# Kernel optimization log

Hardware: AMD Instinct MI355X
Metric: run time of the kernel (lower is better)

Reference implementation:

```python
import jax, jax.numpy as jnp
import numpy as np

D = 512        # model dim
NH = 8         # heads
NL = 4         # layers
MSL = 2048     # max_seq_len for relative positional bias
ITEM_V, CATE_V, SEG_V = 100000, 1000, 2
EPS = 1e-5


def layer_norm(x, w, b):
    mu = jnp.mean(x, axis=-1, keepdims=True)
    var = jnp.mean((x - mu) ** 2, axis=-1, keepdims=True)
    return (x - mu) * jax.lax.rsqrt(var + EPS) * w + b


def setup_inputs() -> dict:
    key = jax.random.key(0)
    ks = jax.random.split(key, 16)
    B, L = 8, 1023
    inp = {
        'historical_item_ids': jax.random.randint(ks[0], (B, L), 0, ITEM_V, dtype=jnp.int32),
        'historical_cate_ids': jax.random.randint(ks[1], (B, L), 0, CATE_V, dtype=jnp.int32),
        'historical_len': jax.random.randint(ks[2], (B,), 0, L, dtype=jnp.int32),
        'target_item_id': jax.random.randint(ks[3], (B,), 0, ITEM_V, dtype=jnp.int32),
        'target_cate_id': jax.random.randint(ks[4], (B,), 0, CATE_V, dtype=jnp.int32),
        # embeddings (init std 0.02 like _init_weights)
        'item_emb': 0.02 * jax.random.normal(ks[5], (ITEM_V, D), jnp.float32),
        'cate_emb': 0.02 * jax.random.normal(ks[6], (CATE_V, D), jnp.float32),
        'seg_emb': 0.02 * jax.random.normal(ks[7], (SEG_V, D), jnp.float32),
        # per-layer stacked params
        'W1': 0.02 * jax.random.normal(ks[8], (NL, D, 4 * D), jnp.float32),
        'b1': jnp.zeros((NL, 4 * D), jnp.float32),
        'W2': 0.02 * jax.random.normal(ks[9], (NL, D, D), jnp.float32),
        'b2': jnp.zeros((NL, D), jnp.float32),
        'ln1_w': jnp.ones((NL, D), jnp.float32), 'ln1_b': jnp.zeros((NL, D), jnp.float32),
        'ln2_w': jnp.ones((NL, D), jnp.float32), 'ln2_b': jnp.zeros((NL, D), jnp.float32),
        'pos_w': 0.02 * jax.random.normal(ks[10], (NL, 2 * MSL - 1), jnp.float32),
        'lnf_w': jnp.ones((D,), jnp.float32), 'lnf_b': jnp.zeros((D,), jnp.float32),
    }
    return inp


def _forward(historical_item_ids, historical_cate_ids, historical_len,
             target_item_id, target_cate_id,
             item_emb, cate_emb, seg_emb, W1, b1, W2, b2,
             ln1_w, ln1_b, ln2_w, ln2_b, pos_w, lnf_w, lnf_b):
    B = historical_item_ids.shape[0]
    ar = jnp.arange(B)
    pad = jnp.zeros((B, 1), historical_item_ids.dtype)
    ids = jnp.concatenate([historical_item_ids, pad], axis=1).at[ar, historical_len].set(target_item_id)
    cids = jnp.concatenate([historical_cate_ids, pad], axis=1).at[ar, historical_len].set(target_cate_id)
    S = ids.shape[1]
    seg = jnp.zeros_like(ids).at[ar, historical_len].set(1)

    h = item_emb[ids] + cate_emb[cids] + seg_emb[seg]  # [B,S,D]

    # relative position bias indices: bias[i,j] = pos_w[MSL-1 + j - i]
    rel_idx = MSL - 1 + jnp.arange(S)[None, :] - jnp.arange(S)[:, None]  # [S,S]
    causal = jnp.tril(jnp.ones((S, S), h.dtype))  # multiplicative mask (mask >= 0)

    for l in range(NL):
        z = jax.nn.silu(h @ W1[l] + b1[l])  # [B,S,4D]
        u, q, k, v = jnp.split(z, 4, axis=-1)
        resh = lambda t: t.reshape(B, S, NH, D // NH).transpose(0, 2, 1, 3)  # [B,H,S,hd]
        u, q, k, v = resh(u), resh(q), resh(k), resh(v)
        bias = pos_w[l][rel_idx]  # [S,S]
        att = jax.nn.silu(jnp.einsum('bhsd,bhtd->bhst', q, k) + bias) * causal
        y = jnp.einsum('bhst,bhtd->bhsd', att, v) * u
        y = y.transpose(0, 2, 1, 3).reshape(B, S, D)
        y = layer_norm(y, ln1_w[l], ln1_b[l])
        y = y @ W2[l] + b2[l]
        h = layer_norm(y + h, ln2_w[l], ln2_b[l])  # dropout p=0 (eval)

    return layer_norm(h, lnf_w, lnf_b)


def reference(historical_item_ids, historical_cate_ids, historical_len,
              target_item_id, target_cate_id,
              item_emb, cate_emb, seg_emb, W1, b1, W2, b2,
              ln1_w, ln1_b, ln2_w, ln2_b, pos_w, lnf_w, lnf_b):
    return _forward(historical_item_ids, historical_cate_ids, historical_len,
                    target_item_id, target_cate_id,
                    item_emb, cate_emb, seg_emb, W1, b1, W2, b2,
                    ln1_w, ln1_b, ln2_w, ln2_b, pos_w, lnf_w, lnf_b)
```

## Files before the change

### kernel.cpp

```cpp
#include <hip/hip_runtime.h>
#include <cstddef>


#define D_MODEL 512
#define S_LEN 1024
#define NHEADS 8

typedef __bf16 bf16x8 __attribute__((ext_vector_type(8)));
typedef float f32x4 __attribute__((ext_vector_type(4)));
typedef unsigned short us4 __attribute__((ext_vector_type(4)));
typedef unsigned short us8 __attribute__((ext_vector_type(8)));

__device__ __forceinline__ float silu_f(float x) {
  return x / (1.f + __expf(-x));
}
__device__ __forceinline__ unsigned short f2bf(float f) {
  unsigned int u = __float_as_uint(f);
  u += 0x7FFF + ((u >> 16) & 1);
  return (unsigned short)(u >> 16);
}
__device__ __forceinline__ float bf2f(unsigned short s) {
  return __uint_as_float(((unsigned int)s) << 16);
}
__device__ __forceinline__ void gll16(const void* g, void* l) {
  __builtin_amdgcn_global_load_lds(
      (const __attribute__((address_space(1))) unsigned int*)g,
      (__attribute__((address_space(3))) unsigned int*)l, 16, 0, 0);
}

__global__ __launch_bounds__(256) void embed_kernel(
    const int* __restrict__ hist_i, const int* __restrict__ hist_c,
    const int* __restrict__ hlen, const int* __restrict__ tgt_i,
    const int* __restrict__ tgt_c, const float* __restrict__ item_emb,
    const float* __restrict__ cate_emb, const float* __restrict__ seg_emb,
    float* __restrict__ h32, unsigned short* __restrict__ hbf) {
  int bs = blockIdx.x;
  int b = bs >> 10, s = bs & 1023;
  int l = hlen[b];
  int id, cid, sg;
  if (s == l)       { id = tgt_i[b]; cid = tgt_c[b]; sg = 1; }
  else if (s < 1023){ id = hist_i[b * 1023 + s]; cid = hist_c[b * 1023 + s]; sg = 0; }
  else              { id = 0; cid = 0; sg = 0; }
  const float* ie = item_emb + (size_t)id * D_MODEL;
  const float* ce = cate_emb + (size_t)cid * D_MODEL;
  const float* se = seg_emb + (size_t)sg * D_MODEL;
  float* hr = h32 + (size_t)bs * D_MODEL;
  unsigned short* hb = hbf + (size_t)bs * D_MODEL;
  for (int d = threadIdx.x; d < D_MODEL; d += 256) {
    float v = ie[d] + ce[d] + se[d];
    hr[d] = v;
    hb[d] = f2bf(v);
  }
}

__global__ __launch_bounds__(256) void transpose_kernel(
    const float* __restrict__ W, unsigned short* __restrict__ Wt,
    int K, int N) {
  const int l = blockIdx.z;
  W += (size_t)l * K * N;
  Wt += (size_t)l * K * N;
  const int n0 = blockIdx.x * 64, k0 = blockIdx.y * 64;
  __shared__ float T[64][65];
  const int tid = threadIdx.x;
  const int rr = tid >> 4, cc = (tid & 15) * 4;
#pragma unroll
  for (int p = 0; p < 4; p++) {
    const int r = rr + p * 16;
    const float4 v = *reinterpret_cast<const float4*>(&W[(size_t)(k0 + r) * N + n0 + cc]);
    T[r][cc] = v.x; T[r][cc + 1] = v.y; T[r][cc + 2] = v.z; T[r][cc + 3] = v.w;
  }
  __syncthreads();
#pragma unroll
  for (int p = 0; p < 4; p++) {
    const int r = rr + p * 16;
    us4 o = { f2bf(T[cc + 0][r]), f2bf(T[cc + 1][r]),
              f2bf(T[cc + 2][r]), f2bf(T[cc + 3][r]) };
    *reinterpret_cast<us4*>(&Wt[(size_t)(n0 + r) * K + k0 + cc]) = o;
  }
}

template <int TM, int TN, int EPI_SILU, typename OutT>
__global__ __launch_bounds__(256) void mfma_gemm(
    const unsigned short* __restrict__ A, const unsigned short* __restrict__ Bt,
    const float* __restrict__ bias, OutT* __restrict__ C,
    int M, int N, int K) {
  constexpr int MI = TM / 32, NI = TN / 32;
  __shared__ unsigned short As[TM * 64];
  __shared__ unsigned short Bs[TN * 64];
  const int tid = threadIdx.x;
  const int w = tid >> 6, lane = tid & 63, lm = lane & 15, quad = lane >> 4;
  const int wm = w & 1, wn = w >> 1;
  const int m0 = blockIdx.y * TM, n0 = blockIdx.x * TN;

  f32x4 acc[MI][NI] = {};

  for (int k0 = 0; k0 < K; k0 += 64) {
#pragma unroll
    for (int p = 0; p < TM / 32; p++) {
      const int g = p * 256 + tid;
      const int r = g >> 3;
      const int lc = (g & 7) ^ (r & 7);
      gll16(A + (size_t)(m0 + r) * K + k0 + lc * 8, &As[g * 8]);
    }
#pragma unroll
    for (int p = 0; p < TN / 32; p++) {
      const int g = p * 256 + tid;
      const int r = g >> 3;
      const int lc = (g & 7) ^ (r & 7);
      gll16(Bt + (size_t)(n0 + r) * K + k0 + lc * 8, &Bs[g * 8]);
    }
    __syncthreads();
#pragma unroll
    for (int ki = 0; ki < 2; ki++) {
      bf16x8 af[MI], bfr[NI];
#pragma unroll
      for (int mi = 0; mi < MI; mi++) {
        const int r = wm * (TM / 2) + mi * 16 + lm;
        const int p = (ki * 4 + quad) ^ (lm & 7);
        af[mi] = *reinterpret_cast<const bf16x8*>(&As[r * 64 + p * 8]);
      }
#pragma unroll
      for (int ni = 0; ni < NI; ni++) {
        const int r = wn * (TN / 2) + ni * 16 + lm;
        const int p = (ki * 4 + quad) ^ (lm & 7);
        bfr[ni] = *reinterpret_cast<const bf16x8*>(&Bs[r * 64 + p * 8]);
      }
#pragma unroll
      for (int mi = 0; mi < MI; mi++)
#pragma unroll
        for (int ni = 0; ni < NI; ni++)
          acc[mi][ni] = __builtin_amdgcn_mfma_f32_16x16x32_bf16(
              af[mi], bfr[ni], acc[mi][ni], 0, 0, 0);
    }
    __syncthreads();
  }

#pragma unroll
  for (int ni = 0; ni < NI; ni++) {
    const int n = n0 + wn * (TN / 2) + ni * 16 + lm;
    const float bv = bias[n];
#pragma unroll
    for (int mi = 0; mi < MI; mi++) {
      const int mbase = m0 + wm * (TM / 2) + mi * 16 + quad * 4;
#pragma unroll
      for (int reg = 0; reg < 4; reg++) {
        float v = acc[mi][ni][reg] + bv;
        if (EPI_SILU) v = silu_f(v);
        if constexpr (sizeof(OutT) == 2)
          C[(size_t)(mbase + reg) * N + n] = f2bf(v);
        else
          C[(size_t)(mbase + reg) * N + n] = v;
      }
    }
  }
}

#define LDR 72
__global__ __launch_bounds__(256) void attn_kernel(
    const unsigned short* __restrict__ z, const float* __restrict__ posw,
    float* __restrict__ y) {
  const int qt = blockIdx.x, hh = blockIdx.y, b = blockIdx.z;
  const int s0 = qt * 128;
  __shared__ alignas(16) unsigned short Qs[128 * LDR];
  __shared__ alignas(16) unsigned short Ps[128 * LDR];
  __shared__ alignas(16) unsigned short Ks[64 * LDR];
  __shared__ alignas(16) unsigned short Vt[64 * LDR];
  __shared__ float bias_s[192];
  const unsigned short* zb = z + (size_t)b * S_LEN * 2048;
  const int tid = threadIdx.x;
  const int w = tid >> 6, lane = tid & 63, lm = lane & 15, quad = lane >> 4;

#pragma unroll
  for (int p = 0; p < 4; p++) {
    const int g = p * 256 + tid;
    const int r = g >> 3, ch = (g & 7) * 8;
    *reinterpret_cast<us8*>(&Qs[r * LDR + ch]) =
        *reinterpret_cast<const us8*>(zb + (size_t)(s0 + r) * 2048 + 512 + hh * 64 + ch);
  }

  f32x4 O[2][4] = {};

  const int ktmax = 2 * qt + 1;
  for (int kt = 0; kt <= ktmax; kt++) {
    const int t0 = kt * 64;
    __syncthreads();
#pragma unroll
    for (int p = 0; p < 2; p++) {
      const int g = p * 256 + tid;
      const int r = g >> 3, ch = (g & 7) * 8;
      *reinterpret_cast<us8*>(&Ks[r * LDR + ch]) =
          *reinterpret_cast<const us8*>(zb + (size_t)(t0 + r) * 2048 + 1024 + hh * 64 + ch);
    }
    {
      const int t = (tid >> 4) * 4;
      const int d = (tid & 15) * 4;
      unsigned short c[4][4];
#pragma unroll
      for (int r = 0; r < 4; r++) {
        const us4 v = *reinterpret_cast<const us4*>(
            zb + (size_t)(t0 + t + r) * 2048 + 1536 + hh * 64 + d);
        c[r][0] = v.x; c[r][1] = v.y; c[r][2] = v.z; c[r][3] = v.w;
      }
      const int tb = t >> 3, ti = t & 7;
#pragma unroll
      for (int j = 0; j < 4; j++) {
        const int dd = d + j;
        us4 o = { c[0][j], c[1][j], c[2][j], c[3][j] };
        *reinterpret_cast<us4*>(&Vt[dd * LDR + ((tb ^ (dd & 7)) << 3) + ti]) = o;
      }
    }
    if (tid < 192) bias_s[tid] = posw[2047 + t0 - s0 - 127 + tid];
    __syncthreads();

#pragma unroll
    for (int mi = 0; mi < 2; mi++) {
      const int qrow = w * 32 + mi * 16;
      const bf16x8 qa0 = *reinterpret_cast<const bf16x8*>(&Qs[(qrow + lm) * LDR + quad * 8]);
      const bf16x8 qa1 = *reinterpret_cast<const bf16x8*>(&Qs[(qrow + lm) * LDR + 32 + quad * 8]);
#pragma unroll
      for (int ct = 0; ct < 4; ct++) {
        const bf16x8 kb0 = *reinterpret_cast<const bf16x8*>(&Ks[(ct * 16 + lm) * LDR + quad * 8]);
        const bf16x8 kb1 = *reinterpret_cast<const bf16x8*>(&Ks[(ct * 16 + lm) * LDR + 32 + quad * 8]);
        f32x4 acc = {};
        acc = __builtin_amdgcn_mfma_f32_16x16x32_bf16(qa0, kb0, acc, 0, 0, 0);
        acc = __builtin_amdgcn_mfma_f32_16x16x32_bf16(qa1, kb1, acc, 0, 0, 0);
        const int bbase = 127 - (qrow + quad * 4);
#pragma unroll
        for (int i = 0; i < 4; i++) {
          const int sg = s0 + qrow + quad * 4 + i;
          const int t = t0 + ct * 16 + lm;
          const float x = acc[i] + bias_s[bbase + ct * 16 + lm - i];
          const float val = (t <= sg) ? silu_f(x) : 0.f;
          Ps[(qrow + quad * 4 + i) * LDR + ct * 16 + lm] = f2bf(val);
        }
      }
    }

    bf16x8 pa0[2], pa1[2];
#pragma unroll
    for (int mi = 0; mi < 2; mi++) {
      const int qrow = w * 32 + mi * 16;
      pa0[mi] = *reinterpret_cast<const bf16x8*>(&Ps[(qrow + lm) * LDR + quad * 8]);
      pa1[mi] = *reinterpret_cast<const bf16x8*>(&Ps[(qrow + lm) * LDR + 32 + quad * 8]);
    }
#pragma unroll
    for (int ct = 0; ct < 4; ct++) {
      const int d = ct * 16 + lm;
      const bf16x8 vb0 = *reinterpret_cast<const bf16x8*>(
          &Vt[d * LDR + ((quad ^ (d & 7)) << 3)]);
      const bf16x8 vb1 = *reinterpret_cast<const bf16x8*>(
          &Vt[d * LDR + (((4 + quad) ^ (d & 7)) << 3)]);
#pragma unroll
      for (int mi = 0; mi < 2; mi++) {
        O[mi][ct] = __builtin_amdgcn_mfma_f32_16x16x32_bf16(pa0[mi], vb0, O[mi][ct], 0, 0, 0);
        O[mi][ct] = __builtin_amdgcn_mfma_f32_16x16x32_bf16(pa1[mi], vb1, O[mi][ct], 0, 0, 0);
      }
    }
  }

#pragma unroll
  for (int mi = 0; mi < 2; mi++) {
    const int srow = s0 + w * 32 + mi * 16 + quad * 4;
#pragma unroll
    for (int ct = 0; ct < 4; ct++) {
      const int d = ct * 16 + lm;
#pragma unroll
      for (int i = 0; i < 4; i++) {
        const int sg = srow + i;
        const float u = bf2f(zb[(size_t)sg * 2048 + hh * 64 + d]);
        y[((size_t)(b * S_LEN + sg)) * D_MODEL + hh * 64 + d] = O[mi][ct][i] * u;
      }
    }
  }
}

__global__ __launch_bounds__(256) void ln_kernel(
    const float* __restrict__ x, const float* __restrict__ res,
    const float* __restrict__ w, const float* __restrict__ bb,
    float* __restrict__ o32, unsigned short* __restrict__ obf) {
  const int wv = threadIdx.x >> 6, lane = threadIdx.x & 63;
  const size_t row = blockIdx.x * 4 + wv;
  const int i0 = lane * 4, i1 = 256 + lane * 4;
  float4 v0 = *reinterpret_cast<const float4*>(&x[row * D_MODEL + i0]);
  float4 v1 = *reinterpret_cast<const float4*>(&x[row * D_MODEL + i1]);
  if (res) {
    const float4 r0 = *reinterpret_cast<const float4*>(&res[row * D_MODEL + i0]);
    const float4 r1 = *reinterpret_cast<const float4*>(&res[row * D_MODEL + i1]);
    v0.x += r0.x; v0.y += r0.y; v0.z += r0.z; v0.w += r0.w;
    v1.x += r1.x; v1.y += r1.y; v1.z += r1.z; v1.w += r1.w;
  }
  float s = v0.x + v0.y + v0.z + v0.w + v1.x + v1.y + v1.z + v1.w;
  float ss = v0.x * v0.x + v0.y * v0.y + v0.z * v0.z + v0.w * v0.w +
             v1.x * v1.x + v1.y * v1.y + v1.z * v1.z + v1.w * v1.w;
#pragma unroll
  for (int off = 32; off; off >>= 1) {
    s += __shfl_down(s, off, 64);
    ss += __shfl_down(ss, off, 64);
  }
  s = __shfl(s, 0, 64);
  ss = __shfl(ss, 0, 64);
  const float mu = s * (1.f / D_MODEL);
  const float rstd = rsqrtf(ss * (1.f / D_MODEL) - mu * mu + 1e-5f);
  const float4 w0 = *reinterpret_cast<const float4*>(&w[i0]);
  const float4 w1 = *reinterpret_cast<const float4*>(&w[i1]);
  const float4 b0 = *reinterpret_cast<const float4*>(&bb[i0]);
  const float4 b1 = *reinterpret_cast<const float4*>(&bb[i1]);
  float r[8];
  r[0] = (v0.x - mu) * rstd * w0.x + b0.x;
  r[1] = (v0.y - mu) * rstd * w0.y + b0.y;
  r[2] = (v0.z - mu) * rstd * w0.z + b0.z;
  r[3] = (v0.w - mu) * rstd * w0.w + b0.w;
  r[4] = (v1.x - mu) * rstd * w1.x + b1.x;
  r[5] = (v1.y - mu) * rstd * w1.y + b1.y;
  r[6] = (v1.z - mu) * rstd * w1.z + b1.z;
  r[7] = (v1.w - mu) * rstd * w1.w + b1.w;
  if (o32) {
    *reinterpret_cast<float4*>(&o32[row * D_MODEL + i0]) = make_float4(r[0], r[1], r[2], r[3]);
    *reinterpret_cast<float4*>(&o32[row * D_MODEL + i1]) = make_float4(r[4], r[5], r[6], r[7]);
  }
  if (obf) {
    us4 q0 = { f2bf(r[0]), f2bf(r[1]), f2bf(r[2]), f2bf(r[3]) };
    us4 q1 = { f2bf(r[4]), f2bf(r[5]), f2bf(r[6]), f2bf(r[7]) };
    *reinterpret_cast<us4*>(&obf[row * D_MODEL + i0]) = q0;
    *reinterpret_cast<us4*>(&obf[row * D_MODEL + i1]) = q1;
  }
}

extern "C" void kernel_launch(void* const* d_in, const int* in_sizes, int n_in,
                              void* d_out, int out_size, void* d_ws, size_t ws_size,
                              hipStream_t stream) {
  const int* hist_i = (const int*)d_in[0];
  const int* hist_c = (const int*)d_in[1];
  const int* hlen   = (const int*)d_in[2];
  const int* tgt_i  = (const int*)d_in[3];
  const int* tgt_c  = (const int*)d_in[4];
  const float* item_emb = (const float*)d_in[5];
  const float* cate_emb = (const float*)d_in[6];
  const float* seg_emb  = (const float*)d_in[7];
  const float* W1   = (const float*)d_in[8];
  const float* b1   = (const float*)d_in[9];
  const float* W2   = (const float*)d_in[10];
  const float* b2   = (const float*)d_in[11];
  const float* ln1w = (const float*)d_in[12];
  const float* ln1b = (const float*)d_in[13];
  const float* ln2w = (const float*)d_in[14];
  const float* ln2b = (const float*)d_in[15];
  const float* posw = (const float*)d_in[16];
  const float* lnfw = (const float*)d_in[17];
  const float* lnfb = (const float*)d_in[18];
  float* out = (float*)d_out;

  char* ws = (char*)d_ws;
  float*          h32 = (float*)(ws);
  unsigned short* hbf = (unsigned short*)(ws + (16u << 20));
  unsigned short* zbf = (unsigned short*)(ws + (24u << 20));
  unsigned short* ybf = (unsigned short*)(ws + (56u << 20));
  float*          yat = (float*)(ws + (64u << 20));
  float*          t32 = yat;
  unsigned short* W1t = (unsigned short*)(ws + (80u << 20));
  unsigned short* W2t = (unsigned short*)(ws + (88u << 20));

  const int ROWS = 8 * S_LEN;

  transpose_kernel<<<dim3(2048 / 64, 512 / 64, 4), 256, 0, stream>>>(W1, W1t, 512, 2048);
  transpose_kernel<<<dim3(512 / 64, 512 / 64, 4), 256, 0, stream>>>(W2, W2t, 512, 512);
  embed_kernel<<<ROWS, 256, 0, stream>>>(hist_i, hist_c, hlen, tgt_i, tgt_c,
                                         item_emb, cate_emb, seg_emb, h32, hbf);
  for (int l = 0; l < 4; l++) {
    mfma_gemm<128, 128, 1, unsigned short><<<dim3(2048 / 128, ROWS / 128), 256, 0, stream>>>(
        hbf, W1t + (size_t)l * 2048 * 512, b1 + (size_t)l * 2048, zbf, ROWS, 2048, 512);
    attn_kernel<<<dim3(S_LEN / 128, NHEADS, 8), 256, 0, stream>>>(
        zbf, posw + (size_t)l * 4095, yat);
    ln_kernel<<<ROWS / 4, 256, 0, stream>>>(yat, nullptr, ln1w + l * 512, ln1b + l * 512,
                                            nullptr, ybf);
    mfma_gemm<64, 64, 0, float><<<dim3(512 / 64, ROWS / 64), 256, 0, stream>>>(
        ybf, W2t + (size_t)l * 512 * 512, b2 + (size_t)l * 512, t32, ROWS, 512, 512);
    ln_kernel<<<ROWS / 4, 256, 0, stream>>>(t32, h32, ln2w + l * 512, ln2b + l * 512,
                                            h32, hbf);
  }
  ln_kernel<<<ROWS / 4, 256, 0, stream>>>(h32, nullptr, lnfw, lnfb, out, nullptr);
}
```

Before: 889.8 us.

## Balance causal attention with paired query tiles and swizzle W1 GEMM blocks per XCD

The attention kernel now handles 64-row query tiles, and each block processes two tiles (qt and 15-qt). This balances causal work across blocks, and Q fragments are held in registers instead of staged in shared memory. Shared memory per block drops, and each wave now owns 16 query rows instead of 32. The first GEMM moves to 256x128 tiles on a 1D grid whose block ids are remapped so blocks sharing an XCD cover neighbouring M rows, aimed at better L2 reuse. The trade-off is less K/V reuse per loaded tile in attention and higher register pressure in the larger GEMM tile.

```diff
diff --git a/kernel.cpp b/kernel.cpp
--- a/kernel.cpp
+++ b/kernel.cpp
@@ -79,7 +79,7 @@
   }
 }
 
-template <int TM, int TN, int EPI_SILU, typename OutT>
+template <int TM, int TN, int SWZ, int EPI_SILU, typename OutT>
 __global__ __launch_bounds__(256) void mfma_gemm(
     const unsigned short* __restrict__ A, const unsigned short* __restrict__ Bt,
     const float* __restrict__ bias, OutT* __restrict__ C,
@@ -90,7 +90,16 @@
   const int tid = threadIdx.x;
   const int w = tid >> 6, lane = tid & 63, lm = lane & 15, quad = lane >> 4;
   const int wm = w & 1, wn = w >> 1;
-  const int m0 = blockIdx.y * TM, n0 = blockIdx.x * TN;
+  int m0, n0;
+  if (SWZ) {
+    const int id = blockIdx.x;
+    const int xcd = id & 7, j = id >> 3;
+    m0 = (xcd * 4 + (j & 3)) * TM;
+    n0 = (j >> 2) * TN;
+  } else {
+    m0 = blockIdx.y * TM;
+    n0 = blockIdx.x * TN;
+  }
 
   f32x4 acc[MI][NI] = {};
 
@@ -159,116 +168,104 @@
 __global__ __launch_bounds__(256) void attn_kernel(
     const unsigned short* __restrict__ z, const float* __restrict__ posw,
     float* __restrict__ y) {
-  const int qt = blockIdx.x, hh = blockIdx.y, b = blockIdx.z;
-  const int s0 = qt * 128;
-  __shared__ alignas(16) unsigned short Qs[128 * LDR];
-  __shared__ alignas(16) unsigned short Ps[128 * LDR];
+  const int hh = blockIdx.y, b = blockIdx.z;
   __shared__ alignas(16) unsigned short Ks[64 * LDR];
   __shared__ alignas(16) unsigned short Vt[64 * LDR];
-  __shared__ float bias_s[192];
+  __shared__ alignas(16) unsigned short Ps[64 * LDR];
+  __shared__ float bias_s[128];
   const unsigned short* zb = z + (size_t)b * S_LEN * 2048;
   const int tid = threadIdx.x;
   const int w = tid >> 6, lane = tid & 63, lm = lane & 15, quad = lane >> 4;
 
 #pragma unroll
-  for (int p = 0; p < 4; p++) {
-    const int g = p * 256 + tid;
-    const int r = g >> 3, ch = (g & 7) * 8;
-    *reinterpret_cast<us8*>(&Qs[r * LDR + ch]) =
-        *reinterpret_cast<const us8*>(zb + (size_t)(s0 + r) * 2048 + 512 + hh * 64 + ch);
-  }
-
-  f32x4 O[2][4] = {};
-
-  const int ktmax = 2 * qt + 1;
-  for (int kt = 0; kt <= ktmax; kt++) {
-    const int t0 = kt * 64;
-    __syncthreads();
-#pragma unroll
-    for (int p = 0; p < 2; p++) {
-      const int g = p * 256 + tid;
-      const int r = g >> 3, ch = (g & 7) * 8;
-      *reinterpret_cast<us8*>(&Ks[r * LDR + ch]) =
-          *reinterpret_cast<const us8*>(zb + (size_t)(t0 + r) * 2048 + 1024 + hh * 64 + ch);
-    }
+  for (int phase = 0; phase < 2; phase++) {
+    const int qt = phase == 0 ? (int)blockIdx.x : 15 - (int)blockIdx.x;
+    const int s0 = qt * 64;
+    const int srow = s0 + w * 16 + lm;
+
+    const bf16x8 qb0 = *reinterpret_cast<const bf16x8*>(
+        zb + (size_t)srow * 2048 + 512 + hh * 64 + quad * 8);
+    const bf16x8 qb1 = *reinterpret_cast<const bf16x8*>(
+        zb + (size_t)srow * 2048 + 512 + hh * 64 + 32 + quad * 8);
+
+    f32x4 O[4] = {};
+
+    for (int kt = 0; kt <= qt; kt++) {
+      const int t0 = kt * 64;
+      __syncthreads();
+#pragma unroll
+      for (int p = 0; p < 2; p++) {
+        const int g = p * 256 + tid;
+        const int r = g >> 3, ch = (g & 7) * 8;
+        *reinterpret_cast<us8*>(&Ks[r * LDR + ch]) =
+            *reinterpret_cast<const us8*>(zb + (size_t)(t0 + r) * 2048 + 1024 + hh * 64 + ch);
+      }
+      {
+        const int t = (tid >> 4) * 4;
+        const int d = (tid & 15) * 4;
+        unsigned short c[4][4];
+#pragma unroll
+        for (int r = 0; r < 4; r++) {
+          const us4 v = *reinterpret_cast<const us4*>(
+              zb + (size_t)(t0 + t + r) * 2048 + 1536 + hh * 64 + d);
+          c[r][0] = v.x; c[r][1] = v.y; c[r][2] = v.z; c[r][3] = v.w;
+        }
+        const int tb = t >> 3, ti = t & 7;
+#pragma unroll
+        for (int j = 0; j < 4; j++) {
+          const int dd = d + j;
+          us4 o = { c[0][j], c[1][j], c[2][j], c[3][j] };
+          *reinterpret_cast<us4*>(&Vt[dd * LDR + ((tb ^ (dd & 7)) << 3) + ti]) = o;
+        }
+      }
+      if (tid < 128) bias_s[tid] = posw[2047 + t0 - s0 - 63 + tid];
+      __syncthreads();
+
+#pragma unroll
+      for (int tt = 0; tt < 4; tt++) {
+        const bf16x8 ka0 = *reinterpret_cast<const bf16x8*>(&Ks[(tt * 16 + lm) * LDR + quad * 8]);
+        const bf16x8 ka1 = *reinterpret_cast<const bf16x8*>(&Ks[(tt * 16 + lm) * LDR + 32 + quad * 8]);
+        f32x4 st = {};
+        st = __builtin_amdgcn_mfma_f32_16x16x32_bf16(ka0, qb0, st, 0, 0, 0);
+        st = __builtin_amdgcn_mfma_f32_16x16x32_bf16(ka1, qb1, st, 0, 0, 0);
+        const int bbase = 63 + tt * 16 + quad * 4 - w * 16 - lm;
+        const int tq = t0 + tt * 16 + quad * 4;
+        us4 pv;
+        unsigned short* pp = (unsigned short*)&pv;
+#pragma unroll
+        for (int i = 0; i < 4; i++) {
+          const float x = st[i] + bias_s[bbase + i];
+          const float val = (tq + i <= srow) ? silu_f(x) : 0.f;
+          pp[i] = f2bf(val);
+        }
+        *reinterpret_cast<us4*>(&Ps[(w * 16 + lm) * LDR + tt * 16 + quad * 4]) = pv;
+      }
+
+      const bf16x8 pa0 = *reinterpret_cast<const bf16x8*>(&Ps[(w * 16 + lm) * LDR + quad * 8]);
+      const bf16x8 pa1 = *reinterpret_cast<const bf16x8*>(&Ps[(w * 16 + lm) * LDR + 32 + quad * 8]);
+#pragma unroll
+      for (int ct = 0; ct < 4; ct++) {
+        const int d = ct * 16 + lm;
+        const bf16x8 vb0 = *reinterpret_cast<const bf16x8*>(
+            &Vt[d * LDR + ((quad ^ (d & 7)) << 3)]);
+        const bf16x8 vb1 = *reinterpret_cast<const bf16x8*>(
+            &Vt[d * LDR + (((4 + quad) ^ (d & 7)) << 3)]);
+        O[ct] = __builtin_amdgcn_mfma_f32_16x16x32_bf16(pa0, vb0, O[ct], 0, 0, 0);
+        O[ct] = __builtin_amdgcn_mfma_f32_16x16x32_bf16(pa1, vb1, O[ct], 0, 0, 0);
+      }
+    }
+
     {
-      const int t = (tid >> 4) * 4;
-      const int d = (tid & 15) * 4;
-      unsigned short c[4][4];
-#pragma unroll
-      for (int r = 0; r < 4; r++) {
-        const us4 v = *reinterpret_cast<const us4*>(
-            zb + (size_t)(t0 + t + r) * 2048 + 1536 + hh * 64 + d);
-        c[r][0] = v.x; c[r][1] = v.y; c[r][2] = v.z; c[r][3] = v.w;
-      }
-      const int tb = t >> 3, ti = t & 7;
-#pragma unroll
-      for (int j = 0; j < 4; j++) {
-        const int dd = d + j;
-        us4 o = { c[0][j], c[1][j], c[2][j], c[3][j] };
-        *reinterpret_cast<us4*>(&Vt[dd * LDR + ((tb ^ (dd & 7)) << 3) + ti]) = o;
-      }
-    }
-    if (tid < 192) bias_s[tid] = posw[2047 + t0 - s0 - 127 + tid];
-    __syncthreads();
-
-#pragma unroll
-    for (int mi = 0; mi < 2; mi++) {
-      const int qrow = w * 32 + mi * 16;
-      const bf16x8 qa0 = *reinterpret_cast<const bf16x8*>(&Qs[(qrow + lm) * LDR + quad * 8]);
-      const bf16x8 qa1 = *reinterpret_cast<const bf16x8*>(&Qs[(qrow + lm) * LDR + 32 + quad * 8]);
+      const int sbase = s0 + w * 16 + quad * 4;
 #pragma unroll
       for (int ct = 0; ct < 4; ct++) {
-        const bf16x8 kb0 = *reinterpret_cast<const bf16x8*>(&Ks[(ct * 16 + lm) * LDR + quad * 8]);
-        const bf16x8 kb1 = *reinterpret_cast<const bf16x8*>(&Ks[(ct * 16 + lm) * LDR + 32 + quad * 8]);
-        f32x4 acc = {};
-        acc = __builtin_amdgcn_mfma_f32_16x16x32_bf16(qa0, kb0, acc, 0, 0, 0);
-        acc = __builtin_amdgcn_mfma_f32_16x16x32_bf16(qa1, kb1, acc, 0, 0, 0);
-        const int bbase = 127 - (qrow + quad * 4);
+        const int d = ct * 16 + lm;
 #pragma unroll
         for (int i = 0; i < 4; i++) {
-          const int sg = s0 + qrow + quad * 4 + i;
-          const int t = t0 + ct * 16 + lm;
-          const float x = acc[i] + bias_s[bbase + ct * 16 + lm - i];
-          const float val = (t <= sg) ? silu_f(x) : 0.f;
-          Ps[(qrow + quad * 4 + i) * LDR + ct * 16 + lm] = f2bf(val);
+          const int sg = sbase + i;
+          const float u = bf2f(zb[(size_t)sg * 2048 + hh * 64 + d]);
+          y[((size_t)(b * S_LEN + sg)) * D_MODEL + hh * 64 + d] = O[ct][i] * u;
         }
-      }
-    }
-
-    bf16x8 pa0[2], pa1[2];
-#pragma unroll
-    for (int mi = 0; mi < 2; mi++) {
-      const int qrow = w * 32 + mi * 16;
-      pa0[mi] = *reinterpret_cast<const bf16x8*>(&Ps[(qrow + lm) * LDR + quad * 8]);
-      pa1[mi] = *reinterpret_cast<const bf16x8*>(&Ps[(qrow + lm) * LDR + 32 + quad * 8]);
-    }
-#pragma unroll
-    for (int ct = 0; ct < 4; ct++) {
-      const int d = ct * 16 + lm;
-      const bf16x8 vb0 = *reinterpret_cast<const bf16x8*>(
-          &Vt[d * LDR + ((quad ^ (d & 7)) << 3)]);
-      const bf16x8 vb1 = *reinterpret_cast<const bf16x8*>(
-          &Vt[d * LDR + (((4 + quad) ^ (d & 7)) << 3)]);
-#pragma unroll
-      for (int mi = 0; mi < 2; mi++) {
-        O[mi][ct] = __builtin_amdgcn_mfma_f32_16x16x32_bf16(pa0[mi], vb0, O[mi][ct], 0, 0, 0);
-        O[mi][ct] = __builtin_amdgcn_mfma_f32_16x16x32_bf16(pa1[mi], vb1, O[mi][ct], 0, 0, 0);
-      }
-    }
-  }
-
-#pragma unroll
-  for (int mi = 0; mi < 2; mi++) {
-    const int srow = s0 + w * 32 + mi * 16 + quad * 4;
-#pragma unroll
-    for (int ct = 0; ct < 4; ct++) {
-      const int d = ct * 16 + lm;
-#pragma unroll
-      for (int i = 0; i < 4; i++) {
-        const int sg = srow + i;
-        const float u = bf2f(zb[(size_t)sg * 2048 + hh * 64 + d]);
-        y[((size_t)(b * S_LEN + sg)) * D_MODEL + hh * 64 + d] = O[mi][ct][i] * u;
       }
     }
   }
@@ -367,13 +364,13 @@
   embed_kernel<<<ROWS, 256, 0, stream>>>(hist_i, hist_c, hlen, tgt_i, tgt_c,
                                          item_emb, cate_emb, seg_emb, h32, hbf);
   for (int l = 0; l < 4; l++) {
-    mfma_gemm<128, 128, 1, unsigned short><<<dim3(2048 / 128, ROWS / 128), 256, 0, stream>>>(
+    mfma_gemm<256, 128, 1, 1, unsigned short><<<512, 256, 0, stream>>>(
         hbf, W1t + (size_t)l * 2048 * 512, b1 + (size_t)l * 2048, zbf, ROWS, 2048, 512);
-    attn_kernel<<<dim3(S_LEN / 128, NHEADS, 8), 256, 0, stream>>>(
+    attn_kernel<<<dim3(8, NHEADS, 8), 256, 0, stream>>>(
         zbf, posw + (size_t)l * 4095, yat);
     ln_kernel<<<ROWS / 4, 256, 0, stream>>>(yat, nullptr, ln1w + l * 512, ln1b + l * 512,
                                             nullptr, ybf);
-    mfma_gemm<64, 64, 0, float><<<dim3(512 / 64, ROWS / 64), 256, 0, stream>>>(
+    mfma_gemm<64, 64, 0, 0, float><<<dim3(512 / 64, ROWS / 64), 256, 0, stream>>>(
         ybf, W2t + (size_t)l * 512 * 512, b2 + (size_t)l * 512, t32, ROWS, 512, 512);
     ln_kernel<<<ROWS / 4, 256, 0, stream>>>(t32, h32, ln2w + l * 512, ln2b + l * 512,
                                             h32, hbf);
```

Measured after the change: 819.2 us. 1.09x faster.
